# Kernel tuning notes

Hardware: AMD Instinct MI355X
Metric: run time of the kernel (lower is better)

The kernel has to match this reference:

```python
import jax, jax.numpy as jnp
import numpy as np

NUM_HEADS = 16

def setup_inputs() -> dict:
    key = jax.random.key(0)
    ks = jax.random.split(key, 5)
    B, T, C = 2, 2048, 1024
    s = 0.02
    return {
        "x": jax.random.normal(ks[0], (B, T, C), dtype=jnp.float32),
        "in_w": jax.random.normal(ks[1], (3 * C, C), dtype=jnp.float32) * s,
        "in_b": jax.random.normal(ks[2], (3 * C,), dtype=jnp.float32) * s,
        "out_w": jax.random.normal(ks[3], (C, C), dtype=jnp.float32) * s,
        "out_b": jax.random.normal(ks[4], (C,), dtype=jnp.float32) * s,
    }

def reference(x, in_w, in_b, out_w, out_b):
    B, T, C = x.shape
    H = NUM_HEADS
    D = C // H
    qvk = x @ in_w.T + in_b  # (B, T, 3C)
    # einops 'b t (d k h) -> k b h t d': factor 3C as (D, 3, H), D outermost
    qvk = qvk.reshape(B, T, D, 3, H).transpose(3, 0, 4, 1, 2)  # (3, B, H, T, D)
    q, v, k = qvk[0], qvk[1], qvk[2]  # note q, v, k assignment order
    scores = jnp.einsum('bhid,bhjd->bhij', q, k) * (D ** -0.5)  # (B, H, T, T)
    causal = jnp.tril(jnp.ones((T, T), dtype=bool))
    scores = jnp.where(causal, scores, -jnp.inf)
    attn = jax.nn.softmax(scores, axis=-1)
    out = jnp.einsum('bhij,bhjd->bhid', attn, v)  # (B, H, T, D)
    out = out.transpose(0, 2, 1, 3).reshape(B, T, C)  # 'b h t d -> b t (h d)'
    return out @ out_w.T + out_b
```

## Files before the change

### kernel.cpp

```cpp
#include <hip/hip_runtime.h>


#define BB 2
#define TT 2048
#define CC 1024
#define HH 16
#define DD 64
#define MM (BB*TT)
#define N3 (3*CC)
#define BH (BB*HH)

typedef unsigned short u16;
typedef unsigned int   u32;
typedef __bf16 bf16x8 __attribute__((ext_vector_type(8)));
typedef float  f32x4  __attribute__((ext_vector_type(4)));

__device__ __forceinline__ u16 f32_to_bf16(float f) {
  u32 u = __float_as_uint(f);
  return (u16)((u + 0x7fffu + ((u >> 16) & 1u)) >> 16);
}
__device__ __forceinline__ u16 f32_to_bf16_fast(float f) {
  return (u16)((__float_as_uint(f) + 0x8000u) >> 16);
}
__device__ __forceinline__ u32 pack2_bf16(float a, float b) {
  u32 ua = __float_as_uint(a) + 0x8000u;
  u32 ub = __float_as_uint(b) + 0x8000u;
  return __builtin_amdgcn_perm(ub, ua, 0x07060302);
}

#define N4_X  (MM * CC / 4)
#define N4_W  (N3 * CC / 4)
#define N4_OW (CC * CC / 4)
__global__ __launch_bounds__(256) void cast_all(const float* __restrict__ x,
                                                const float* __restrict__ in_w,
                                                const float* __restrict__ out_w,
                                                u16* __restrict__ xb,
                                                u16* __restrict__ wb,
                                                u16* __restrict__ owb) {
  int i = blockIdx.x * 256 + threadIdx.x;
  const float* src; u16* dst; int j;
  if (i < N4_X)            { src = x;     dst = xb;  j = i; }
  else if (i < N4_X + N4_W){ src = in_w;  dst = wb;  j = i - N4_X; }
  else                     { src = out_w; dst = owb; j = i - N4_X - N4_W; }
  float4 f = reinterpret_cast<const float4*>(src)[j];
  uint2 pk;
  pk.x = (u32)f32_to_bf16(f.x) | ((u32)f32_to_bf16(f.y) << 16);
  pk.y = (u32)f32_to_bf16(f.z) | ((u32)f32_to_bf16(f.w) << 16);
  reinterpret_cast<uint2*>(dst)[j] = pk;
}

__device__ __forceinline__ void gemm_core(const u16* __restrict__ Ag,
                                          const u16* __restrict__ Bg,
                                          int K, u16* Al, u16* Bl,
                                          int m0, int n0, f32x4 acc[4][4]) {
  const int tid = threadIdx.x, lane = tid & 63, w = tid >> 6;
  const int quad = lane >> 4, colr = lane & 15;
  const int mw = (w >> 1) * 64, nw = (w & 1) * 64;
  const int srow = lane >> 3, scol = lane & 7;
  const uint4* Al4 = reinterpret_cast<const uint4*>(Al);
  const uint4* Bl4 = reinterpret_cast<const uint4*>(Bl);
  for (int kt = 0; kt < K / 64; ++kt) {
    __syncthreads();
    #pragma unroll
    for (int ii = 0; ii < 4; ++ii) {
      int inst = w * 4 + ii;
      int row = inst * 8 + srow;
      int cs = scol ^ (row & 7);
      const u16* ga = Ag + (size_t)(m0 + row) * K + kt * 64 + cs * 8;
      const u16* gb = Bg + (size_t)(n0 + row) * K + kt * 64 + cs * 8;
      __builtin_amdgcn_global_load_lds(
          (const __attribute__((address_space(1))) void*)ga,
          (__attribute__((address_space(3))) void*)(Al + inst * 512), 16, 0, 0);
      __builtin_amdgcn_global_load_lds(
          (const __attribute__((address_space(1))) void*)gb,
          (__attribute__((address_space(3))) void*)(Bl + inst * 512), 16, 0, 0);
    }
    __syncthreads();
    #pragma unroll
    for (int ks = 0; ks < 2; ++ks) {
      bf16x8 af[4], bfr[4];
      #pragma unroll
      for (int t = 0; t < 4; ++t) {
        int mrow = mw + t * 16 + colr;
        af[t]  = __builtin_bit_cast(bf16x8, Al4[mrow * 8 + ((ks * 4 + quad) ^ (mrow & 7))]);
        int nrow = nw + t * 16 + colr;
        bfr[t] = __builtin_bit_cast(bf16x8, Bl4[nrow * 8 + ((ks * 4 + quad) ^ (nrow & 7))]);
      }
      #pragma unroll
      for (int mt = 0; mt < 4; ++mt)
        #pragma unroll
        for (int nt = 0; nt < 4; ++nt)
          acc[mt][nt] = __builtin_amdgcn_mfma_f32_16x16x32_bf16(af[mt], bfr[nt], acc[mt][nt], 0, 0, 0);
    }
  }
}

__global__ __launch_bounds__(256) void gemm_qkv(const u16* __restrict__ xb,
                                                const u16* __restrict__ wb,
                                                const float* __restrict__ in_b,
                                                u16* __restrict__ Y) {
  __shared__ __align__(16) u16 Al[128 * 64];
  __shared__ __align__(16) u16 Bl[128 * 64];
  const int lane = threadIdx.x & 63, w = threadIdx.x >> 6;
  const int quad = lane >> 4, colr = lane & 15;
  const int mw = (w >> 1) * 64, nw = (w & 1) * 64;
  const int m0 = blockIdx.x * 128, n0 = blockIdx.y * 128;
  f32x4 acc[4][4];
  #pragma unroll
  for (int mt = 0; mt < 4; ++mt)
    #pragma unroll
    for (int nt = 0; nt < 4; ++nt) acc[mt][nt] = (f32x4){0.f, 0.f, 0.f, 0.f};
  gemm_core(xb, wb, CC, Al, Bl, m0, n0, acc);
  float bias[4];
  #pragma unroll
  for (int nt = 0; nt < 4; ++nt) bias[nt] = in_b[n0 + nw + nt * 16 + colr];
  #pragma unroll
  for (int mt = 0; mt < 4; ++mt)
    #pragma unroll
    for (int e = 0; e < 4; ++e) {
      int row = m0 + mw + mt * 16 + quad * 4 + e;
      #pragma unroll
      for (int nt = 0; nt < 4; ++nt)
        Y[(size_t)row * N3 + n0 + nw + nt * 16 + colr] = f32_to_bf16(acc[mt][nt][e] + bias[nt]);
    }
}

__global__ __launch_bounds__(256) void repack_qkv(const u16* __restrict__ Y,
                                                  u16* __restrict__ qkv) {
  __shared__ __align__(16) u16 Yl[N3];
  const int m = blockIdx.x, tid = threadIdx.x;
  const int b_ = m >> 11, t = m & (TT - 1);
  const uint4* Yg = reinterpret_cast<const uint4*>(Y + (size_t)m * N3);
  uint4* Yl4 = reinterpret_cast<uint4*>(Yl);
  for (int i = tid; i < N3 / 8; i += 256) Yl4[i] = Yg[i];
  __syncthreads();
  for (int it = tid; it < 768; it += 256) {
    int h = it & 15, s = (it >> 4) % 3, dg = it / 48;
    int col = s * 16 + h;
    u32 lo = (u32)Yl[(dg * 4 + 0) * 48 + col] | ((u32)Yl[(dg * 4 + 1) * 48 + col] << 16);
    u32 hi = (u32)Yl[(dg * 4 + 2) * 48 + col] | ((u32)Yl[(dg * 4 + 3) * 48 + col] << 16);
    uint2 pk; pk.x = lo; pk.y = hi;
    size_t base = (((size_t)s * BH + b_ * HH + h) * TT + t) * DD + dg * 4;
    *reinterpret_cast<uint2*>(qkv + base) = pk;
  }
}

__global__ __launch_bounds__(256, 2) void attn_mfma(const u16* __restrict__ qkv,
                                                    u16* __restrict__ aout) {
  __shared__ __align__(16) u32   Vt[2][64 * 36];
  __shared__ __align__(16) float Pl[4 * 32 * 68];
  const int tid  = threadIdx.x;
  const int lane = tid & 63, w = tid >> 6;
  const int quad = lane >> 4, colr = lane & 15;
  const int flat = blockIdx.x;
  const int bh = (flat & 7) * 4 + (flat >> 7);
  const int qt = 15 - ((flat >> 3) & 15);
  const int b_ = bh >> 4, h = bh & 15;
  const int i0 = qt * 128;
  const int jmax = 2 * qt + 1;

  const uint4* Qg4 = reinterpret_cast<const uint4*>(qkv + (size_t)bh * TT * DD);
  const uint4* Vg4 = reinterpret_cast<const uint4*>(qkv + ((size_t)BH + bh) * TT * DD);
  const uint4* Kg4 = reinterpret_cast<const uint4*>(qkv + ((size_t)2 * BH + bh) * TT * DD);
  const float4* Pl4 = reinterpret_cast<const float4*>(Pl);

  const int s_jp = tid & 31, s_oct = tid >> 5;
  const int wbase = w * (32 * 68);

  bf16x8 qa[2][2];
  #pragma unroll
  for (int u = 0; u < 2; ++u)
    #pragma unroll
    for (int ks = 0; ks < 2; ++ks)
      qa[u][ks] = __builtin_bit_cast(bf16x8,
          Qg4[(size_t)(i0 + w * 32 + u * 16 + colr) * 8 + ks * 4 + quad]);

  f32x4 oacc[2][4];
  #pragma unroll
  for (int u = 0; u < 2; ++u)
    #pragma unroll
    for (int dt = 0; dt < 4; ++dt) oacc[u][dt] = (f32x4){0.f, 0.f, 0.f, 0.f};
  float lp[2] = {0.f, 0.f};

  uint4 va = Vg4[(size_t)(2 * s_jp) * 8 + s_oct];
  uint4 vb = Vg4[(size_t)(2 * s_jp + 1) * 8 + s_oct];

  for (int jt = 0; jt <= jmax; ++jt) {
    const int j0 = jt * 64;
    u32* vtw = Vt[jt & 1];
    const uint4* vt4 = reinterpret_cast<const uint4*>(Vt[jt & 1]);

    uint4 kraw[4][2];
    #pragma unroll
    for (int t4 = 0; t4 < 4; ++t4)
      #pragma unroll
      for (int ks = 0; ks < 2; ++ks)
        kraw[t4][ks] = Kg4[(size_t)(j0 + t4 * 16 + colr) * 8 + ks * 4 + quad];

    {
      u32 aw[4] = {va.x, va.y, va.z, va.w};
      u32 bw[4] = {vb.x, vb.y, vb.z, vb.w};
      #pragma unroll
      for (int m = 0; m < 4; ++m) {
        vtw[(s_oct * 8 + 2 * m)     * 36 + s_jp] = __builtin_amdgcn_perm(bw[m], aw[m], 0x05040100);
        vtw[(s_oct * 8 + 2 * m + 1) * 36 + s_jp] = __builtin_amdgcn_perm(bw[m], aw[m], 0x07060302);
      }
    }
    if (jt < jmax) {
      int nj = j0 + 64;
      va = Vg4[(size_t)(nj + 2 * s_jp) * 8 + s_oct];
      vb = Vg4[(size_t)(nj + 2 * s_jp + 1) * 8 + s_oct];
    }
    __syncthreads();

    f32x4 sacc[2][4];
    #pragma unroll
    for (int u = 0; u < 2; ++u)
      #pragma unroll
      for (int t4 = 0; t4 < 4; ++t4) sacc[u][t4] = (f32x4){0.f, 0.f, 0.f, 0.f};
    #pragma unroll
    for (int t4 = 0; t4 < 4; ++t4)
      #pragma unroll
      for (int ks = 0; ks < 2; ++ks) {
        bf16x8 kb = __builtin_bit_cast(bf16x8, kraw[t4][ks]);
        #pragma unroll
        for (int u = 0; u < 2; ++u)
          sacc[u][t4] = __builtin_amdgcn_mfma_f32_16x16x32_bf16(qa[u][ks], kb, sacc[u][t4], 0, 0, 0);
      }

    const bool maskt = (jt >= 2 * qt);
    const int joff = (jt - 2 * qt) * 64;
    #pragma unroll
    for (int u = 0; u < 2; ++u)
      #pragma unroll
      for (int t4 = 0; t4 < 4; ++t4)
        #pragma unroll
        for (int rg = 0; rg < 4; ++rg) {
          float p = __builtin_amdgcn_exp2f(sacc[u][t4][rg] * 0.18033688011112042f);
          if (maskt && (joff + t4 * 16 + colr > w * 32 + u * 16 + quad * 4 + rg)) p = 0.f;
          Pl[wbase + (u * 16 + quad * 4 + rg) * 68 + t4 * 16 + colr] = p;
        }

    bf16x8 pa[2][2];
    #pragma unroll
    for (int u = 0; u < 2; ++u)
      #pragma unroll
      for (int ks = 0; ks < 2; ++ks) {
        int b4 = (wbase + (u * 16 + colr) * 68 + ks * 32 + quad * 8) >> 2;
        float4 f0 = Pl4[b4], f1 = Pl4[b4 + 1];
        lp[u] += ((f0.x + f0.y) + (f0.z + f0.w)) + ((f1.x + f1.y) + (f1.z + f1.w));
        uint4 up;
        up.x = pack2_bf16(f0.x, f0.y); up.y = pack2_bf16(f0.z, f0.w);
        up.z = pack2_bf16(f1.x, f1.y); up.w = pack2_bf16(f1.z, f1.w);
        pa[u][ks] = __builtin_bit_cast(bf16x8, up);
      }

    #pragma unroll
    for (int dt = 0; dt < 4; ++dt)
      #pragma unroll
      for (int ks = 0; ks < 2; ++ks) {
        bf16x8 vfr = __builtin_bit_cast(bf16x8, vt4[(dt * 16 + colr) * 9 + ks * 4 + quad]);
        #pragma unroll
        for (int u = 0; u < 2; ++u)
          oacc[u][dt] = __builtin_amdgcn_mfma_f32_16x16x32_bf16(pa[u][ks], vfr, oacc[u][dt], 0, 0, 0);
      }
  }

  #pragma unroll
  for (int u = 0; u < 2; ++u) {
    float ls = lp[u];
    ls += __shfl_xor(ls, 16);
    ls += __shfl_xor(ls, 32);
    float linv[4];
    #pragma unroll
    for (int rg = 0; rg < 4; ++rg)
      linv[rg] = 1.0f / __shfl(ls, quad * 4 + rg);
    #pragma unroll
    for (int dt = 0; dt < 4; ++dt)
      #pragma unroll
      for (int rg = 0; rg < 4; ++rg) {
        int ig = i0 + w * 32 + u * 16 + quad * 4 + rg;
        size_t off = ((size_t)(b_ * TT + ig)) * CC + h * DD + dt * 16 + colr;
        aout[off] = f32_to_bf16_fast(oacc[u][dt][rg] * linv[rg]);
      }
  }
}

__global__ __launch_bounds__(256) void gemm_out(const u16* __restrict__ ab,
                                                const u16* __restrict__ owb,
                                                const float* __restrict__ out_b,
                                                float* __restrict__ out) {
  __shared__ __align__(16) u16 Al[128 * 64];
  __shared__ __align__(16) u16 Bl[128 * 64];
  const int lane = threadIdx.x & 63, w = threadIdx.x >> 6;
  const int quad = lane >> 4, colr = lane & 15;
  const int mw = (w >> 1) * 64, nw = (w & 1) * 64;
  const int m0 = blockIdx.x * 128, n0 = blockIdx.y * 128;
  f32x4 acc[4][4];
  #pragma unroll
  for (int mt = 0; mt < 4; ++mt)
    #pragma unroll
    for (int nt = 0; nt < 4; ++nt) acc[mt][nt] = (f32x4){0.f, 0.f, 0.f, 0.f};
  gemm_core(ab, owb, CC, Al, Bl, m0, n0, acc);
  float bias[4];
  #pragma unroll
  for (int nt = 0; nt < 4; ++nt) bias[nt] = out_b[n0 + nw + nt * 16 + colr];
  #pragma unroll
  for (int mt = 0; mt < 4; ++mt)
    #pragma unroll
    for (int e = 0; e < 4; ++e) {
      int row = m0 + mw + mt * 16 + quad * 4 + e;
      #pragma unroll
      for (int nt = 0; nt < 4; ++nt)
        out[(size_t)row * CC + n0 + nw + nt * 16 + colr] = acc[mt][nt][e] + bias[nt];
    }
}

extern "C" void kernel_launch(void* const* d_in, const int* in_sizes, int n_in,
                              void* d_out, int out_size, void* d_ws, size_t ws_size,
                              hipStream_t stream) {
  const float* x     = (const float*)d_in[0];
  const float* in_w  = (const float*)d_in[1];
  const float* in_b  = (const float*)d_in[2];
  const float* out_w = (const float*)d_in[3];
  const float* out_b = (const float*)d_in[4];
  float* out = (float*)d_out;

  char* ws = (char*)d_ws;
  u16* xb  = (u16*)(ws + 0);
  u16* ab  = (u16*)(ws + 0);
  u16* wb  = (u16*)(ws + 8388608);
  u16* owb = (u16*)(ws + 14680064);
  u16* Y   = (u16*)(ws + 16777216);
  u16* qkv = (u16*)(ws + 41943040);

  cast_all<<<dim3((N4_X + N4_W + N4_OW) / 256), 256, 0, stream>>>(x, in_w, out_w, xb, wb, owb);

  gemm_qkv<<<dim3(MM / 128, N3 / 128), 256, 0, stream>>>(xb, wb, in_b, Y);
  repack_qkv<<<dim3(MM), 256, 0, stream>>>(Y, qkv);
  attn_mfma<<<dim3(512), 256, 0, stream>>>(qkv, ab);
  gemm_out<<<dim3(MM / 128, CC / 128), 256, 0, stream>>>(ab, owb, out_b, out);
}
```

Before: 250.3 us.

## Pair short and long causal query tiles per block to balance attention work

The attention kernel now uses 128-thread blocks, each handling two 64-row query tiles, pr and 31-pr, in sequence. Every block therefore does about the same total number of key tiles, which is meant to remove the load imbalance of the causal triangle. V staging is widened so each thread loads two octets. The cost is fewer waves per block, serial passes with an extra barrier, and a different occupancy picture with the launch-bounds min-blocks hint removed.

```diff
diff --git a/kernel.cpp b/kernel.cpp
--- a/kernel.cpp
+++ b/kernel.cpp
@@ -145,144 +145,157 @@
   }
 }
 
-__global__ __launch_bounds__(256, 2) void attn_mfma(const u16* __restrict__ qkv,
-                                                    u16* __restrict__ aout) {
+__global__ __launch_bounds__(128) void attn_mfma(const u16* __restrict__ qkv,
+                                                 u16* __restrict__ aout) {
   __shared__ __align__(16) u32   Vt[2][64 * 36];
-  __shared__ __align__(16) float Pl[4 * 32 * 68];
+  __shared__ __align__(16) float Pl[2 * 32 * 68];
   const int tid  = threadIdx.x;
   const int lane = tid & 63, w = tid >> 6;
   const int quad = lane >> 4, colr = lane & 15;
   const int flat = blockIdx.x;
   const int bh = (flat & 7) * 4 + (flat >> 7);
-  const int qt = 15 - ((flat >> 3) & 15);
+  const int pr = (flat >> 3) & 15;
   const int b_ = bh >> 4, h = bh & 15;
-  const int i0 = qt * 128;
-  const int jmax = 2 * qt + 1;
 
   const uint4* Qg4 = reinterpret_cast<const uint4*>(qkv + (size_t)bh * TT * DD);
   const uint4* Vg4 = reinterpret_cast<const uint4*>(qkv + ((size_t)BH + bh) * TT * DD);
   const uint4* Kg4 = reinterpret_cast<const uint4*>(qkv + ((size_t)2 * BH + bh) * TT * DD);
   const float4* Pl4 = reinterpret_cast<const float4*>(Pl);
 
-  const int s_jp = tid & 31, s_oct = tid >> 5;
+  const int s_jp = tid & 31, s_half = tid >> 5;
   const int wbase = w * (32 * 68);
 
-  bf16x8 qa[2][2];
-  #pragma unroll
-  for (int u = 0; u < 2; ++u)
-    #pragma unroll
-    for (int ks = 0; ks < 2; ++ks)
-      qa[u][ks] = __builtin_bit_cast(bf16x8,
-          Qg4[(size_t)(i0 + w * 32 + u * 16 + colr) * 8 + ks * 4 + quad]);
-
-  f32x4 oacc[2][4];
-  #pragma unroll
-  for (int u = 0; u < 2; ++u)
-    #pragma unroll
-    for (int dt = 0; dt < 4; ++dt) oacc[u][dt] = (f32x4){0.f, 0.f, 0.f, 0.f};
-  float lp[2] = {0.f, 0.f};
-
-  uint4 va = Vg4[(size_t)(2 * s_jp) * 8 + s_oct];
-  uint4 vb = Vg4[(size_t)(2 * s_jp + 1) * 8 + s_oct];
-
-  for (int jt = 0; jt <= jmax; ++jt) {
-    const int j0 = jt * 64;
-    u32* vtw = Vt[jt & 1];
-    const uint4* vt4 = reinterpret_cast<const uint4*>(Vt[jt & 1]);
-
-    uint4 kraw[4][2];
-    #pragma unroll
-    for (int t4 = 0; t4 < 4; ++t4)
+  for (int pass = 0; pass < 2; ++pass) {
+    const int qt = pass ? (31 - pr) : pr;
+    const int i0 = qt * 64;
+    const int jmax = qt;
+
+    bf16x8 qa[2][2];
+    #pragma unroll
+    for (int u = 0; u < 2; ++u)
       #pragma unroll
       for (int ks = 0; ks < 2; ++ks)
-        kraw[t4][ks] = Kg4[(size_t)(j0 + t4 * 16 + colr) * 8 + ks * 4 + quad];
-
-    {
-      u32 aw[4] = {va.x, va.y, va.z, va.w};
-      u32 bw[4] = {vb.x, vb.y, vb.z, vb.w};
-      #pragma unroll
-      for (int m = 0; m < 4; ++m) {
-        vtw[(s_oct * 8 + 2 * m)     * 36 + s_jp] = __builtin_amdgcn_perm(bw[m], aw[m], 0x05040100);
-        vtw[(s_oct * 8 + 2 * m + 1) * 36 + s_jp] = __builtin_amdgcn_perm(bw[m], aw[m], 0x07060302);
+        qa[u][ks] = __builtin_bit_cast(bf16x8,
+            Qg4[(size_t)(i0 + w * 32 + u * 16 + colr) * 8 + ks * 4 + quad]);
+
+    f32x4 oacc[2][4];
+    #pragma unroll
+    for (int u = 0; u < 2; ++u)
+      #pragma unroll
+      for (int dt = 0; dt < 4; ++dt) oacc[u][dt] = (f32x4){0.f, 0.f, 0.f, 0.f};
+    float lp[2] = {0.f, 0.f};
+
+    uint4 va[2], vb[2];
+    #pragma unroll
+    for (int io = 0; io < 2; ++io) {
+      va[io] = Vg4[(size_t)(2 * s_jp) * 8 + s_half + io * 4];
+      vb[io] = Vg4[(size_t)(2 * s_jp + 1) * 8 + s_half + io * 4];
+    }
+
+    for (int jt = 0; jt <= jmax; ++jt) {
+      const int j0 = jt * 64;
+      u32* vtw = Vt[jt & 1];
+      const uint4* vt4 = reinterpret_cast<const uint4*>(Vt[jt & 1]);
+
+      uint4 kraw[4][2];
+      #pragma unroll
+      for (int t4 = 0; t4 < 4; ++t4)
+        #pragma unroll
+        for (int ks = 0; ks < 2; ++ks)
+          kraw[t4][ks] = Kg4[(size_t)(j0 + t4 * 16 + colr) * 8 + ks * 4 + quad];
+
+      #pragma unroll
+      for (int io = 0; io < 2; ++io) {
+        const int oc = s_half + io * 4;
+        u32 aw[4] = {va[io].x, va[io].y, va[io].z, va[io].w};
+        u32 bw[4] = {vb[io].x, vb[io].y, vb[io].z, vb[io].w};
+        #pragma unroll
+        for (int m = 0; m < 4; ++m) {
+          vtw[(oc * 8 + 2 * m)     * 36 + s_jp] = __builtin_amdgcn_perm(bw[m], aw[m], 0x05040100);
+          vtw[(oc * 8 + 2 * m + 1) * 36 + s_jp] = __builtin_amdgcn_perm(bw[m], aw[m], 0x07060302);
+        }
       }
-    }
-    if (jt < jmax) {
-      int nj = j0 + 64;
-      va = Vg4[(size_t)(nj + 2 * s_jp) * 8 + s_oct];
-      vb = Vg4[(size_t)(nj + 2 * s_jp + 1) * 8 + s_oct];
+      if (jt < jmax) {
+        int nj = j0 + 64;
+        #pragma unroll
+        for (int io = 0; io < 2; ++io) {
+          va[io] = Vg4[(size_t)(nj + 2 * s_jp) * 8 + s_half + io * 4];
+          vb[io] = Vg4[(size_t)(nj + 2 * s_jp + 1) * 8 + s_half + io * 4];
+        }
+      }
+      __syncthreads();
+
+      f32x4 sacc[2][4];
+      #pragma unroll
+      for (int u = 0; u < 2; ++u)
+        #pragma unroll
+        for (int t4 = 0; t4 < 4; ++t4) sacc[u][t4] = (f32x4){0.f, 0.f, 0.f, 0.f};
+      #pragma unroll
+      for (int t4 = 0; t4 < 4; ++t4)
+        #pragma unroll
+        for (int ks = 0; ks < 2; ++ks) {
+          bf16x8 kb = __builtin_bit_cast(bf16x8, kraw[t4][ks]);
+          #pragma unroll
+          for (int u = 0; u < 2; ++u)
+            sacc[u][t4] = __builtin_amdgcn_mfma_f32_16x16x32_bf16(qa[u][ks], kb, sacc[u][t4], 0, 0, 0);
+        }
+
+      const bool maskt = (jt == qt);
+      #pragma unroll
+      for (int u = 0; u < 2; ++u)
+        #pragma unroll
+        for (int t4 = 0; t4 < 4; ++t4)
+          #pragma unroll
+          for (int rg = 0; rg < 4; ++rg) {
+            float p = __builtin_amdgcn_exp2f(sacc[u][t4][rg] * 0.18033688011112042f);
+            if (maskt && (t4 * 16 + colr > w * 32 + u * 16 + quad * 4 + rg)) p = 0.f;
+            Pl[wbase + (u * 16 + quad * 4 + rg) * 68 + t4 * 16 + colr] = p;
+          }
+
+      bf16x8 pa[2][2];
+      #pragma unroll
+      for (int u = 0; u < 2; ++u)
+        #pragma unroll
+        for (int ks = 0; ks < 2; ++ks) {
+          int b4 = (wbase + (u * 16 + colr) * 68 + ks * 32 + quad * 8) >> 2;
+          float4 f0 = Pl4[b4], f1 = Pl4[b4 + 1];
+          lp[u] += ((f0.x + f0.y) + (f0.z + f0.w)) + ((f1.x + f1.y) + (f1.z + f1.w));
+          uint4 up;
+          up.x = pack2_bf16(f0.x, f0.y); up.y = pack2_bf16(f0.z, f0.w);
+          up.z = pack2_bf16(f1.x, f1.y); up.w = pack2_bf16(f1.z, f1.w);
+          pa[u][ks] = __builtin_bit_cast(bf16x8, up);
+        }
+
+      #pragma unroll
+      for (int dt = 0; dt < 4; ++dt)
+        #pragma unroll
+        for (int ks = 0; ks < 2; ++ks) {
+          bf16x8 vfr = __builtin_bit_cast(bf16x8, vt4[(dt * 16 + colr) * 9 + ks * 4 + quad]);
+          #pragma unroll
+          for (int u = 0; u < 2; ++u)
+            oacc[u][dt] = __builtin_amdgcn_mfma_f32_16x16x32_bf16(pa[u][ks], vfr, oacc[u][dt], 0, 0, 0);
+        }
+    }
+
+    #pragma unroll
+    for (int u = 0; u < 2; ++u) {
+      float ls = lp[u];
+      ls += __shfl_xor(ls, 16);
+      ls += __shfl_xor(ls, 32);
+      float linv[4];
+      #pragma unroll
+      for (int rg = 0; rg < 4; ++rg)
+        linv[rg] = 1.0f / __shfl(ls, quad * 4 + rg);
+      #pragma unroll
+      for (int dt = 0; dt < 4; ++dt)
+        #pragma unroll
+        for (int rg = 0; rg < 4; ++rg) {
+          int ig = i0 + w * 32 + u * 16 + quad * 4 + rg;
+          size_t off = ((size_t)(b_ * TT + ig)) * CC + h * DD + dt * 16 + colr;
+          aout[off] = f32_to_bf16_fast(oacc[u][dt][rg] * linv[rg]);
+        }
     }
     __syncthreads();
-
-    f32x4 sacc[2][4];
-    #pragma unroll
-    for (int u = 0; u < 2; ++u)
-      #pragma unroll
-      for (int t4 = 0; t4 < 4; ++t4) sacc[u][t4] = (f32x4){0.f, 0.f, 0.f, 0.f};
-    #pragma unroll
-    for (int t4 = 0; t4 < 4; ++t4)
-      #pragma unroll
-      for (int ks = 0; ks < 2; ++ks) {
-        bf16x8 kb = __builtin_bit_cast(bf16x8, kraw[t4][ks]);
-        #pragma unroll
-        for (int u = 0; u < 2; ++u)
-          sacc[u][t4] = __builtin_amdgcn_mfma_f32_16x16x32_bf16(qa[u][ks], kb, sacc[u][t4], 0, 0, 0);
-      }
-
-    const bool maskt = (jt >= 2 * qt);
-    const int joff = (jt - 2 * qt) * 64;
-    #pragma unroll
-    for (int u = 0; u < 2; ++u)
-      #pragma unroll
-      for (int t4 = 0; t4 < 4; ++t4)
-        #pragma unroll
-        for (int rg = 0; rg < 4; ++rg) {
-          float p = __builtin_amdgcn_exp2f(sacc[u][t4][rg] * 0.18033688011112042f);
-          if (maskt && (joff + t4 * 16 + colr > w * 32 + u * 16 + quad * 4 + rg)) p = 0.f;
-          Pl[wbase + (u * 16 + quad * 4 + rg) * 68 + t4 * 16 + colr] = p;
-        }
-
-    bf16x8 pa[2][2];
-    #pragma unroll
-    for (int u = 0; u < 2; ++u)
-      #pragma unroll
-      for (int ks = 0; ks < 2; ++ks) {
-        int b4 = (wbase + (u * 16 + colr) * 68 + ks * 32 + quad * 8) >> 2;
-        float4 f0 = Pl4[b4], f1 = Pl4[b4 + 1];
-        lp[u] += ((f0.x + f0.y) + (f0.z + f0.w)) + ((f1.x + f1.y) + (f1.z + f1.w));
-        uint4 up;
-        up.x = pack2_bf16(f0.x, f0.y); up.y = pack2_bf16(f0.z, f0.w);
-        up.z = pack2_bf16(f1.x, f1.y); up.w = pack2_bf16(f1.z, f1.w);
-        pa[u][ks] = __builtin_bit_cast(bf16x8, up);
-      }
-
-    #pragma unroll
-    for (int dt = 0; dt < 4; ++dt)
-      #pragma unroll
-      for (int ks = 0; ks < 2; ++ks) {
-        bf16x8 vfr = __builtin_bit_cast(bf16x8, vt4[(dt * 16 + colr) * 9 + ks * 4 + quad]);
-        #pragma unroll
-        for (int u = 0; u < 2; ++u)
-          oacc[u][dt] = __builtin_amdgcn_mfma_f32_16x16x32_bf16(pa[u][ks], vfr, oacc[u][dt], 0, 0, 0);
-      }
-  }
-
-  #pragma unroll
-  for (int u = 0; u < 2; ++u) {
-    float ls = lp[u];
-    ls += __shfl_xor(ls, 16);
-    ls += __shfl_xor(ls, 32);
-    float linv[4];
-    #pragma unroll
-    for (int rg = 0; rg < 4; ++rg)
-      linv[rg] = 1.0f / __shfl(ls, quad * 4 + rg);
-    #pragma unroll
-    for (int dt = 0; dt < 4; ++dt)
-      #pragma unroll
-      for (int rg = 0; rg < 4; ++rg) {
-        int ig = i0 + w * 32 + u * 16 + quad * 4 + rg;
-        size_t off = ((size_t)(b_ * TT + ig)) * CC + h * DD + dt * 16 + colr;
-        aout[off] = f32_to_bf16_fast(oacc[u][dt][rg] * linv[rg]);
-      }
   }
 }
 
@@ -338,6 +351,6 @@
 
   gemm_qkv<<<dim3(MM / 128, N3 / 128), 256, 0, stream>>>(xb, wb, in_b, Y);
   repack_qkv<<<dim3(MM), 256, 0, stream>>>(Y, qkv);
-  attn_mfma<<<dim3(512), 256, 0, stream>>>(qkv, ab);
+  attn_mfma<<<dim3(512), 128, 0, stream>>>(qkv, ab);
   gemm_out<<<dim3(MM / 128, CC / 128), 256, 0, stream>>>(ab, owb, out_b, out);
 }
```

Result: faster. 226.2 us (-9.6%).
